# Kernel tuning notes

Measured on AMD Instinct MI355X. Metric: run time of the kernel, lower is better.

Reference implementation:

```python
import jax, jax.numpy as jnp
import numpy as np

EMBED = 1024
HEADS = 16
HEAD_DIM = EMBED // HEADS


def setup_inputs() -> dict:
    key = jax.random.key(0)
    k1, k2, k3 = jax.random.split(key, 3)
    B, T = 4, 2048
    query = jax.random.normal(k1, (B, T, EMBED), dtype=jnp.float32)
    # xavier-ish scaled weights
    in_proj_w = jax.random.normal(k2, (3 * EMBED, EMBED), dtype=jnp.float32) * (1.0 / np.sqrt(EMBED))
    in_proj_b = jnp.zeros((3 * EMBED,), dtype=jnp.float32)
    out_proj_w = jax.random.normal(k3, (EMBED, EMBED), dtype=jnp.float32) * (1.0 / np.sqrt(EMBED))
    out_proj_b = jnp.zeros((EMBED,), dtype=jnp.float32)
    return {"query": query, "in_proj_w": in_proj_w, "in_proj_b": in_proj_b,
            "out_proj_w": out_proj_w, "out_proj_b": out_proj_b}


def reference(query, in_proj_w, in_proj_b, out_proj_w, out_proj_b):
    # Self-attention (qkv_same path), batch_first=True, dropout=0 (eval).
    B, T, E = query.shape
    H, D = HEADS, HEAD_DIM
    scaling = D ** -0.5
    # fused QKV projection: [B,T,3E]
    qkv = jnp.einsum('bte,fe->btf', query, in_proj_w) + in_proj_b
    q, k, v = jnp.split(qkv, 3, axis=-1)
    q = q * scaling
    # reshape to [B,H,T,D]
    q = q.reshape(B, T, H, D).transpose(0, 2, 1, 3)
    k = k.reshape(B, T, H, D).transpose(0, 2, 1, 3)
    v = v.reshape(B, T, H, D).transpose(0, 2, 1, 3)
    scores = jnp.einsum('bhqd,bhkd->bhqk', q, k)
    attn = jax.nn.softmax(scores, axis=-1)
    ctx = jnp.einsum('bhqk,bhkd->bhqd', attn, v)  # [B,H,T,D]
    ctx = ctx.transpose(0, 2, 1, 3).reshape(B, T, E)
    out = jnp.einsum('bte,fe->btf', ctx, out_proj_w) + out_proj_b
    return out
```

## Files before the change

kernel.cpp:

```cpp
#include <hip/hip_runtime.h>
#include <math.h>

using bf16x8 = __attribute__((ext_vector_type(8))) short;
using f32x4  = __attribute__((ext_vector_type(4))) float;
using u16x8  = __attribute__((ext_vector_type(8))) unsigned short;
using u16x4  = __attribute__((ext_vector_type(4))) unsigned short;

constexpr int Bb = 4, Tt = 2048, Ee = 1024, Hh = 16;
constexpr int Mm = Bb * Tt;
constexpr int E3 = 3 * Ee;

__device__ __forceinline__ unsigned short f2bf(float f) {
  union { float f; unsigned int u; } c; c.f = f;
  unsigned int u = c.u;
  u += 0x7fffu + ((u >> 16) & 1u);
  return (unsigned short)(u >> 16);
}

__device__ __forceinline__ f32x4 mfma16(bf16x8 a, bf16x8 b, f32x4 c) {
  return __builtin_amdgcn_mfma_f32_16x16x32_bf16(a, b, c, 0, 0, 0);
}

__device__ __forceinline__ void gload_lds16(const unsigned short* g, unsigned short* l) {
  __builtin_amdgcn_global_load_lds(
      (const __attribute__((address_space(1))) unsigned int*)g,
      (__attribute__((address_space(3))) unsigned int*)l, 16, 0, 0);
}

__global__ void cvt_f32_bf16(const float* __restrict__ in, unsigned short* __restrict__ out, int n8) {
  const int i = blockIdx.x * 256 + threadIdx.x;
  if (i >= n8) return;
  const float4* p = (const float4*)in + (size_t)i * 2;
  const float4 a = p[0], b = p[1];
  u16x8 r = { f2bf(a.x), f2bf(a.y), f2bf(a.z), f2bf(a.w),
              f2bf(b.x), f2bf(b.y), f2bf(b.z), f2bf(b.w) };
  *(u16x8*)(out + (size_t)i * 8) = r;
}

template <bool OUT_BF16, bool QSCALE>
__global__ __launch_bounds__(256, 2)
void gemm_bt(const unsigned short* __restrict__ A, const unsigned short* __restrict__ Bw,
             const float* __restrict__ bias, void* __restrict__ Cout, int N, int K) {
  __shared__ alignas(16) unsigned short As[128 * 32];
  __shared__ alignas(16) unsigned short Bs[128 * 32];
  const int tid = threadIdx.x;
  const int wave = tid >> 6, lane = tid & 63;
  const int l15 = lane & 15, quad = lane >> 4;
  const int wr = wave >> 1, wc = wave & 1;
  const int row0 = blockIdx.y * 128, col0 = blockIdx.x * 128;
  const int srow = lane >> 2, sslot = lane & 3;

  f32x4 acc[4][4];
#pragma unroll
  for (int i = 0; i < 4; ++i)
#pragma unroll
    for (int j = 0; j < 4; ++j) acc[i][j] = f32x4{0.f, 0.f, 0.f, 0.f};

  for (int k0 = 0; k0 < K; k0 += 32) {
#pragma unroll
    for (int t = 0; t < 2; ++t) {
      const int rA = wave * 32 + t * 16 + srow;
      const int g = sslot ^ ((rA >> 1) & 3);
      gload_lds16(A  + (size_t)(row0 + rA) * K + k0 + g * 8, &As[(wave * 32 + t * 16) * 32]);
      gload_lds16(Bw + (size_t)(col0 + rA) * K + k0 + g * 8, &Bs[(wave * 32 + t * 16) * 32]);
    }
    __syncthreads();

    bf16x8 af[4], bfr[4];
#pragma unroll
    for (int mi = 0; mi < 4; ++mi) {
      const int m = wr * 64 + mi * 16 + l15;
      af[mi] = *(const bf16x8*)&As[m * 32 + (quad ^ ((m >> 1) & 3)) * 8];
    }
#pragma unroll
    for (int ni = 0; ni < 4; ++ni) {
      const int n = wc * 64 + ni * 16 + l15;
      bfr[ni] = *(const bf16x8*)&Bs[n * 32 + (quad ^ ((n >> 1) & 3)) * 8];
    }
#pragma unroll
    for (int mi = 0; mi < 4; ++mi)
#pragma unroll
      for (int ni = 0; ni < 4; ++ni) acc[mi][ni] = mfma16(af[mi], bfr[ni], acc[mi][ni]);
    __syncthreads();
  }

#pragma unroll
  for (int mi = 0; mi < 4; ++mi)
#pragma unroll
    for (int ni = 0; ni < 4; ++ni) {
      const int col = col0 + wc * 64 + ni * 16 + l15;
      const float bv = bias[col];
      const float scale = (QSCALE && col < 1024) ? 0.18033688f : 1.0f;
#pragma unroll
      for (int r = 0; r < 4; ++r) {
        const int row = row0 + wr * 64 + mi * 16 + quad * 4 + r;
        float v = (acc[mi][ni][r] + bv) * scale;
        if (OUT_BF16)
          ((unsigned short*)Cout)[(size_t)row * N + col] = f2bf(v);
        else
          ((float*)Cout)[(size_t)row * N + col] = v;
      }
    }
}

__global__ __launch_bounds__(256, 2)
void transpose_v(const unsigned short* __restrict__ qkv, unsigned short* __restrict__ vt) {
  __shared__ unsigned short L[128][66];
  const int tid = threadIdx.x;
  const int bh = blockIdx.x, b = bh >> 4, h = bh & 15;
  const int t0 = blockIdx.y * 128;
#pragma unroll
  for (int p = 0; p < 8; ++p) {
    const int tl = p * 16 + (tid >> 4);
    const int d = (tid & 15) * 4;
    *(u16x4*)&L[tl][d] = *(const u16x4*)(qkv + (size_t)(b * Tt + t0 + tl) * E3 + 2 * Ee + h * 64 + d);
  }
  __syncthreads();
#pragma unroll
  for (int p = 0; p < 8; ++p) {
    const int dw = (tid >> 5) * 8 + p;
    const int tw = (tid & 31) * 4;
    u16x4 w = { L[tw][dw], L[tw + 1][dw], L[tw + 2][dw], L[tw + 3][dw] };
    *(u16x4*)(vt + ((size_t)bh * 64 + dw) * Tt + t0 + tw) = w;
  }
}

__global__ __launch_bounds__(256, 2)
void attn_mfma2(const unsigned short* __restrict__ qkv,
                const unsigned short* __restrict__ vt,
                unsigned short* __restrict__ ctx) {
  __shared__ alignas(16) unsigned short Ps[4 * 4096];
  const int tid = threadIdx.x;
  const int wave = tid >> 6, lane = tid & 63;
  const int l15 = lane & 15, quad = lane >> 4;
  const int bh = blockIdx.x, b = bh >> 4, h = bh & 15;
  const int q0 = blockIdx.y * 256 + wave * 64;
  unsigned short* const ps = &Ps[wave * 4096];
  const int swz = l15 & 14;

  bf16x8 qa[4][2];
#pragma unroll
  for (int qi = 0; qi < 4; ++qi)
#pragma unroll
    for (int kf = 0; kf < 2; ++kf)
      qa[qi][kf] = *(const bf16x8*)(qkv +
          (size_t)(b * Tt + q0 + qi * 16 + l15) * E3 + h * 64 + kf * 32 + quad * 8);

  f32x4 o[4][4], ol[4];
#pragma unroll
  for (int qi = 0; qi < 4; ++qi) {
    ol[qi] = f32x4{0.f, 0.f, 0.f, 0.f};
#pragma unroll
    for (int di = 0; di < 4; ++di) o[qi][di] = f32x4{0.f, 0.f, 0.f, 0.f};
  }
  bf16x8 ones;
#pragma unroll
  for (int i = 0; i < 8; ++i) ones[i] = (short)0x3F80;

  const unsigned short* kp = qkv + (size_t)(b * Tt + l15) * E3 + Ee + h * 64 + quad * 8;
  const unsigned short* vp = vt + ((size_t)bh * 64 + l15) * Tt + quad * 8;

  for (int it = 0; it < Tt / 64; ++it) {
    bf16x8 vb[4][2], kb[4][2];
#pragma unroll
    for (int di = 0; di < 4; ++di)
#pragma unroll
      for (int kf = 0; kf < 2; ++kf)
        vb[di][kf] = *(const bf16x8*)(vp + di * 16 * Tt + kf * 32);
#pragma unroll
    for (int ki = 0; ki < 4; ++ki)
#pragma unroll
      for (int kf = 0; kf < 2; ++kf)
        kb[ki][kf] = *(const bf16x8*)(kp + (size_t)ki * 16 * E3 + kf * 32);

#pragma unroll
    for (int ki = 0; ki < 4; ++ki) {
      f32x4 s[4];
#pragma unroll
      for (int qi = 0; qi < 4; ++qi) {
        s[qi] = mfma16(kb[ki][0], qa[qi][0], f32x4{0.f, 0.f, 0.f, 0.f});
        s[qi] = mfma16(kb[ki][1], qa[qi][1], s[qi]);
      }
#pragma unroll
      for (int qi = 0; qi < 4; ++qi) {
        const float e0 = __builtin_amdgcn_exp2f(s[qi][0]);
        const float e1 = __builtin_amdgcn_exp2f(s[qi][1]);
        const float e2 = __builtin_amdgcn_exp2f(s[qi][2]);
        const float e3 = __builtin_amdgcn_exp2f(s[qi][3]);
        uint2 w;
        w.x = __builtin_amdgcn_perm(__float_as_uint(e1), __float_as_uint(e0), 0x07060302u);
        w.y = __builtin_amdgcn_perm(__float_as_uint(e3), __float_as_uint(e2), 0x07060302u);
        *(uint2*)(ps + (qi * 16 + l15) * 64 + (((ki * 4 + quad) ^ swz) << 2)) = w;
      }
    }
    __asm__ volatile("s_waitcnt lgkmcnt(0)" ::: "memory");

    bf16x8 pa[4][2];
#pragma unroll
    for (int qi = 0; qi < 4; ++qi)
#pragma unroll
      for (int kf = 0; kf < 2; ++kf)
        pa[qi][kf] = *(const bf16x8*)(ps + (qi * 16 + l15) * 64 + (((kf * 8 + quad * 2) ^ swz) << 2));
#pragma unroll
    for (int qi = 0; qi < 4; ++qi) {
      ol[qi] = mfma16(pa[qi][0], ones, ol[qi]);
      ol[qi] = mfma16(pa[qi][1], ones, ol[qi]);
#pragma unroll
      for (int di = 0; di < 4; ++di) {
        o[qi][di] = mfma16(pa[qi][0], vb[di][0], o[qi][di]);
        o[qi][di] = mfma16(pa[qi][1], vb[di][1], o[qi][di]);
      }
    }
    kp += 64 * E3;
    vp += 64;
  }

#pragma unroll
  for (int qi = 0; qi < 4; ++qi) {
    f32x4 inv;
#pragma unroll
    for (int r = 0; r < 4; ++r) inv[r] = 1.0f / ol[qi][r];
#pragma unroll
    for (int di = 0; di < 4; ++di)
#pragma unroll
      for (int r = 0; r < 4; ++r)
        ctx[(size_t)(b * Tt + q0 + qi * 16 + quad * 4 + r) * Ee + h * 64 + di * 16 + l15] =
            f2bf(o[qi][di][r] * inv[r]);
  }
}

extern "C" void kernel_launch(void* const* d_in, const int* in_sizes, int n_in,
                              void* d_out, int out_size, void* d_ws, size_t ws_size,
                              hipStream_t stream) {
  const float* query = (const float*)d_in[0];
  const float* in_w  = (const float*)d_in[1];
  const float* in_b  = (const float*)d_in[2];
  const float* out_w = (const float*)d_in[3];
  const float* out_b = (const float*)d_in[4];
  float* out = (float*)d_out;

  char* w = (char*)d_ws;
  unsigned short* qkvb = (unsigned short*)(w);
  unsigned short* ctxb = (unsigned short*)(w + 50331648);
  unsigned short* qb   = (unsigned short*)(w + 67108864);
  unsigned short* wib  = (unsigned short*)(w + 83886080);
  unsigned short* wob  = (unsigned short*)(w + 90177536);
  unsigned short* vtb  = (unsigned short*)(w + 92274688);

  cvt_f32_bf16<<<4096, 256, 0, stream>>>(query, qb, (Mm * Ee) / 8);
  cvt_f32_bf16<<<1536, 256, 0, stream>>>(in_w, wib, (E3 * Ee) / 8);
  cvt_f32_bf16<<<512, 256, 0, stream>>>(out_w, wob, (Ee * Ee) / 8);

  gemm_bt<true, true><<<dim3(E3 / 128, Mm / 128), 256, 0, stream>>>(qb, wib, in_b, qkvb, E3, Ee);
  transpose_v<<<dim3(Bb * Hh, Tt / 128), 256, 0, stream>>>(qkvb, vtb);
  attn_mfma2<<<dim3(Bb * Hh, Tt / 256), 256, 0, stream>>>(qkvb, vtb, ctxb);
  gemm_bt<false, false><<<dim3(Ee / 128, Mm / 128), 256, 0, stream>>>(ctxb, wob, out_b, out, Ee, Ee);
}
```

Baseline: 317.9 us.

## Split attention key range across wave pairs and fuse conversion launches

The attention kernel now assigns two waves to each 64-query tile, each covering half of the key sequence. The partial outputs and row sums are merged through LDS before normalisation, and the grid doubles to 128 queries per block, raising parallelism and occupancy. The three fp32-to-bf16 conversion launches are merged into one kernel to cut launch overhead. The cost is one extra LDS exchange with two barriers, and a larger shared buffer per block.

```diff
diff --git a/kernel.cpp b/kernel.cpp
--- a/kernel.cpp
+++ b/kernel.cpp
@@ -27,9 +27,16 @@
       (__attribute__((address_space(3))) unsigned int*)l, 16, 0, 0);
 }
 
-__global__ void cvt_f32_bf16(const float* __restrict__ in, unsigned short* __restrict__ out, int n8) {
-  const int i = blockIdx.x * 256 + threadIdx.x;
-  if (i >= n8) return;
+__global__ void cvt_all(const float* __restrict__ q, const float* __restrict__ iw,
+                        const float* __restrict__ ow, unsigned short* __restrict__ qb,
+                        unsigned short* __restrict__ wib, unsigned short* __restrict__ wob) {
+  constexpr int nQ = Mm * Ee / 8, nI = E3 * Ee / 8, nO = Ee * Ee / 8;
+  int i = blockIdx.x * 256 + threadIdx.x;
+  const float* in; unsigned short* out;
+  if (i < nQ) { in = q; out = qb; }
+  else if (i < nQ + nI) { in = iw; out = wib; i -= nQ; }
+  else if (i < nQ + nI + nO) { in = ow; out = wob; i -= nQ + nI; }
+  else return;
   const float4* p = (const float4*)in + (size_t)i * 2;
   const float4 a = p[0], b = p[1];
   u16x8 r = { f2bf(a.x), f2bf(a.y), f2bf(a.z), f2bf(a.w),
@@ -125,17 +132,18 @@
   }
 }
 
-__global__ __launch_bounds__(256, 2)
-void attn_mfma2(const unsigned short* __restrict__ qkv,
+__global__ __launch_bounds__(256, 4)
+void attn_mfma3(const unsigned short* __restrict__ qkv,
                 const unsigned short* __restrict__ vt,
                 unsigned short* __restrict__ ctx) {
-  __shared__ alignas(16) unsigned short Ps[4 * 4096];
+  __shared__ alignas(16) char lds[40960];
   const int tid = threadIdx.x;
   const int wave = tid >> 6, lane = tid & 63;
   const int l15 = lane & 15, quad = lane >> 4;
+  const int pair = wave >> 1, kh = wave & 1;
   const int bh = blockIdx.x, b = bh >> 4, h = bh & 15;
-  const int q0 = blockIdx.y * 256 + wave * 64;
-  unsigned short* const ps = &Ps[wave * 4096];
+  const int q0 = blockIdx.y * 128 + pair * 64;
+  unsigned short* const ps = (unsigned short*)lds + wave * 4096;
   const int swz = l15 & 14;
 
   bf16x8 qa[4][2];
@@ -157,10 +165,11 @@
 #pragma unroll
   for (int i = 0; i < 8; ++i) ones[i] = (short)0x3F80;
 
-  const unsigned short* kp = qkv + (size_t)(b * Tt + l15) * E3 + Ee + h * 64 + quad * 8;
-  const unsigned short* vp = vt + ((size_t)bh * 64 + l15) * Tt + quad * 8;
-
-  for (int it = 0; it < Tt / 64; ++it) {
+  const unsigned short* kp =
+      qkv + (size_t)(b * Tt + kh * 1024 + l15) * E3 + Ee + h * 64 + quad * 8;
+  const unsigned short* vp = vt + ((size_t)bh * 64 + l15) * Tt + kh * 1024 + quad * 8;
+
+  for (int it = 0; it < 16; ++it) {
     bf16x8 vb[4][2], kb[4][2];
 #pragma unroll
     for (int di = 0; di < 4; ++di)
@@ -215,17 +224,33 @@
     vp += 64;
   }
 
-#pragma unroll
-  for (int qi = 0; qi < 4; ++qi) {
-    f32x4 inv;
-#pragma unroll
-    for (int r = 0; r < 4; ++r) inv[r] = 1.0f / ol[qi][r];
-#pragma unroll
-    for (int di = 0; di < 4; ++di)
-#pragma unroll
-      for (int r = 0; r < 4; ++r)
-        ctx[(size_t)(b * Tt + q0 + qi * 16 + quad * 4 + r) * Ee + h * 64 + di * 16 + l15] =
-            f2bf(o[qi][di][r] * inv[r]);
+  __syncthreads();
+  f32x4* const ex = (f32x4*)lds + (size_t)pair * 1280;
+  if (kh == 1) {
+#pragma unroll
+    for (int qi = 0; qi < 4; ++qi) {
+#pragma unroll
+      for (int di = 0; di < 4; ++di) ex[(qi * 4 + di) * 64 + lane] = o[qi][di];
+      ex[(16 + qi) * 64 + lane] = ol[qi];
+    }
+  }
+  __syncthreads();
+  if (kh == 0) {
+#pragma unroll
+    for (int qi = 0; qi < 4; ++qi) {
+      const f32x4 l2 = ex[(16 + qi) * 64 + lane];
+      f32x4 inv;
+#pragma unroll
+      for (int r = 0; r < 4; ++r) inv[r] = 1.0f / (ol[qi][r] + l2[r]);
+#pragma unroll
+      for (int di = 0; di < 4; ++di) {
+        const f32x4 o2 = ex[(qi * 4 + di) * 64 + lane];
+#pragma unroll
+        for (int r = 0; r < 4; ++r)
+          ctx[(size_t)(b * Tt + q0 + qi * 16 + quad * 4 + r) * Ee + h * 64 + di * 16 + l15] =
+              f2bf((o[qi][di][r] + o2[r]) * inv[r]);
+      }
+    }
   }
 }
 
@@ -247,12 +272,9 @@
   unsigned short* wob  = (unsigned short*)(w + 90177536);
   unsigned short* vtb  = (unsigned short*)(w + 92274688);
 
-  cvt_f32_bf16<<<4096, 256, 0, stream>>>(query, qb, (Mm * Ee) / 8);
-  cvt_f32_bf16<<<1536, 256, 0, stream>>>(in_w, wib, (E3 * Ee) / 8);
-  cvt_f32_bf16<<<512, 256, 0, stream>>>(out_w, wob, (Ee * Ee) / 8);
-
+  cvt_all<<<6144, 256, 0, stream>>>(query, in_w, out_w, qb, wib, wob);
   gemm_bt<true, true><<<dim3(E3 / 128, Mm / 128), 256, 0, stream>>>(qb, wib, in_b, qkvb, E3, Ee);
   transpose_v<<<dim3(Bb * Hh, Tt / 128), 256, 0, stream>>>(qkvb, vtb);
-  attn_mfma2<<<dim3(Bb * Hh, Tt / 256), 256, 0, stream>>>(qkvb, vtb, ctxb);
+  attn_mfma3<<<dim3(Bb * Hh, Tt / 128), 256, 0, stream>>>(qkvb, vtb, ctxb);
   gemm_bt<false, false><<<dim3(Ee / 128, Mm / 128), 256, 0, stream>>>(ctxb, wob, out_b, out, Ee, Ee);
 }
```

Result: slower. 575.5 us (+81.0%).
